# Performance work log

Measured on AMD Instinct MI355X. Metric: run time of the kernel, lower is better.

The kernel has to match this reference:

```python
import jax, jax.numpy as jnp
import numpy as np
import math

B, S, H, DK, NB = 2, 128, 4, 128, 4
D = H * DK  # 512


def setup_inputs() -> dict:
    key = jax.random.key(0)
    ks = jax.random.split(key, 24)
    g = lambda i, sh, std=1.0: jax.random.normal(ks[i], sh, jnp.float32) * std
    u = lambda i, sh: jax.random.uniform(ks[i], sh, jnp.float32)
    return {
        "x_m": g(0, (B, S, D)), "x_c": g(1, (B, S, D)),
        "b_m": g(2, (B, S, D)), "b_c": g(3, (B, S, D)),
        "bb_m": g(4, (B, NB, NB, D)), "bb_c": u(5, (B, NB, NB, D)),
        "p_m": g(6, (B, S, D)), "p_c": u(7, (B, S, D)),
        "W_xm": g(8, (3, D, H, DK), 0.02), "W_xc": g(9, (3, D, H, DK), 0.02),
        "W_bm": g(10, (3, D, H, DK), 0.02), "W_bc": g(11, (3, D, H, DK), 0.02),
        "Wq1_w": g(12, (DK, DK), 0.05), "Wq1_b": g(13, (DK,), 0.02),
        "Wq2_w": g(14, (DK, DK), 0.05), "Wq2_b": g(15, (DK,), 0.02),
        "Wk1_w": g(16, (DK, DK), 0.05), "Wk1_b": g(17, (DK,), 0.02),
        "Wk2_w": g(18, (DK, DK), 0.05), "Wk2_b": g(19, (DK,), 0.02),
        "mean_w": g(20, (D, D), 0.02), "mean_b": jnp.zeros((D,), jnp.float32),
        "cov_w": g(21, (D, D), 0.02), "cov_b": jnp.zeros((D,), jnp.float32),
        "ln_w": jnp.ones((D,), jnp.float32), "ln_b": jnp.zeros((D,), jnp.float32),
        "b_seq": jax.random.randint(ks[22], (B, S), 0, NB),
    }


def _elu1(x):
    return jax.nn.elu(x) + 1.0


def _tri_sagp(m1, m2, m3, c1, c2, c3):
    # fuse three diagonal Gaussians by product-of-Gaussians (precision-weighted)
    eps = 1e-24
    p1 = 1.0 / jnp.clip(c1, eps)
    p2 = 1.0 / jnp.clip(c2, eps)
    p3 = 1.0 / jnp.clip(c3, eps)
    c = 1.0 / (p1 + p2 + p3)
    return c * (m1 * p1 + m2 * p2 + m3 * p3), c


def _ln(x, w, b):
    m = jnp.mean(x, -1, keepdims=True)
    v = jnp.mean((x - m) ** 2, -1, keepdims=True)
    return (x - m) / jnp.sqrt(v + 1e-12) * w + b


def _forward(x_m, x_c, b_m, b_c, bb_m, bb_c, p_m, p_c,
             W_xm, W_xc, W_bm, W_bc,
             Wq1_w, Wq1_b, Wq2_w, Wq2_b, Wk1_w, Wk1_b, Wk2_w, Wk2_b,
             mean_w, mean_b, cov_w, cov_b, ln_w, ln_b, b_seq):
    Bb, Ss, Dd = x_m.shape
    Hh, Dk = W_xm.shape[2], W_xm.shape[3]
    proj = lambda x, w: jnp.einsum('bnd,dhk->bhnk', x, w)
    q1 = proj(x_m, W_xm[0]) + proj(b_m, W_bm[0])
    k1 = proj(x_m, W_xm[1]) + proj(b_m, W_bm[1])
    v1 = proj(x_m, W_xm[2]) + proj(b_m, W_bm[2])
    q2 = _elu1(proj(x_c, W_xc[0]) + proj(b_c, W_bc[0]))
    k2 = _elu1(proj(x_c, W_xc[1]) + proj(b_c, W_bc[1]))
    v2 = _elu1(proj(x_c, W_xc[2]) + proj(b_c, W_bc[2]))
    nb = bb_m.shape[1]
    # [B,NB,NB,D] -> [B,H,NB,NB,DK]
    bbm = bb_m.reshape(Bb, nb, nb, Hh, Dk).transpose(0, 3, 1, 2, 4)
    bbc = bb_c.reshape(Bb, nb, nb, Hh, Dk).transpose(0, 3, 1, 2, 4)
    # out[b,h,i,j,:] = bbm[b,h,b_seq[b,j],b_seq[b,i],:]  (matches torch advanced indexing + permute)
    gather = jax.vmap(lambda bb, seq: bb[:, seq[None, :], seq[:, None], :])
    bbm_b = gather(bbm, b_seq)  # [B,H,S,S,DK]
    bbc_b = gather(bbc, b_seq)
    pm = p_m.reshape(Bb, Ss, Hh, Dk).transpose(0, 2, 1, 3)  # [B,H,S,DK]
    pc = p_c.reshape(Bb, Ss, Hh, Dk).transpose(0, 2, 1, 3)
    lin = lambda x, w, b: x @ w.T + b
    fQm, fQc = _tri_sagp(q1[:, :, :, None, :], lin(bbm_b, Wq1_w, Wq1_b),
                         lin(pm, Wq2_w, Wq2_b)[:, :, :, None, :],
                         q2[:, :, :, None, :], bbc_b, pc[:, :, :, None, :])
    fKm, fKc = _tri_sagp(k1[:, :, None, :, :], lin(bbm_b, Wk1_w, Wk1_b),
                         lin(pm, Wk2_w, Wk2_b)[:, :, None, :, :],
                         k2[:, :, None, :, :], bbc_b, pc[:, :, None, :, :])
    eps = 1e-24
    # 2-Wasserstein^2 between diagonal Gaussians (the 1x1 matmul form reduces to this)
    w2 = jnp.sum((fQm - fKm) ** 2, -1) + jnp.sum(
        (jnp.sqrt(jnp.clip(fQc, eps)) - jnp.sqrt(jnp.clip(fKc, eps))) ** 2, -1)
    scores = -w2 / math.sqrt(Dk)  # [B,H,S,S]
    probs = jax.nn.softmax(scores, axis=-1)
    mean_ctx = jnp.einsum('bhij,bhjk->bhik', probs, v1)
    cov_ctx = jnp.einsum('bhij,bhjk->bhik', probs ** 2, v2)
    mean_ctx = mean_ctx.transpose(0, 2, 1, 3).reshape(Bb, Ss, Dd)
    cov_ctx = cov_ctx.transpose(0, 2, 1, 3).reshape(Bb, Ss, Dd)
    mean_h = _ln(mean_ctx @ mean_w.T + mean_b + x_m, ln_w, ln_b)
    cov_h = _ln(cov_ctx @ cov_w.T + cov_b + x_c, ln_w, ln_b)
    return mean_h, cov_h, probs


def reference(x_m, x_c, b_m, b_c, bb_m, bb_c, p_m, p_c,
              W_xm, W_xc, W_bm, W_bc,
              Wq1_w, Wq1_b, Wq2_w, Wq2_b, Wk1_w, Wk1_b, Wk2_w, Wk2_b,
              mean_w, mean_b, cov_w, cov_b, ln_w, ln_b, b_seq):
    return _forward(x_m, x_c, b_m, b_c, bb_m, bb_c, p_m, p_c,
                    W_xm, W_xc, W_bm, W_bc,
                    Wq1_w, Wq1_b, Wq2_w, Wq2_b, Wk1_w, Wk1_b, Wk2_w, Wk2_b,
                    mean_w, mean_b, cov_w, cov_b, ln_w, ln_b, b_seq)
```

## Files before the change

### kernel.cpp

```cpp
#include <hip/hip_runtime.h>
#include <math.h>

#define B_ 2
#define S_ 128
#define H_ 4
#define DK_ 128
#define NB_ 4
#define D_ 512
#define M_ 256

typedef __attribute__((ext_vector_type(8))) short short8;
typedef __attribute__((ext_vector_type(4))) float float4v;
typedef __attribute__((ext_vector_type(4))) unsigned short ushort4v;

__device__ __forceinline__ float elu1(float x) {
    return (x > 0.f) ? (x + 1.f) : __expf(x);
}

__device__ __forceinline__ unsigned short f2bf(float f) {
    unsigned u = __float_as_uint(f);
    unsigned r = (u + 0x7FFFu + ((u >> 16) & 1u)) >> 16;
    return (unsigned short)r;
}


__global__ __launch_bounds__(256) void k_prep(
    const float* __restrict__ x_m, const float* __restrict__ b_m,
    const float* __restrict__ x_c, const float* __restrict__ b_c,
    const float* __restrict__ mean_w, const float* __restrict__ cov_w,
    const float* __restrict__ W_xm, const float* __restrict__ W_xc,
    const float* __restrict__ W_bm, const float* __restrict__ W_bc,
    const float* __restrict__ p_m, const float* __restrict__ bb_m,
    const float* __restrict__ Wq2, const float* __restrict__ Wk2,
    const float* __restrict__ Wq1, const float* __restrict__ Wk1,
    unsigned short* __restrict__ A_m, unsigned short* __restrict__ A_c,
    unsigned short* __restrict__ wm_bf, unsigned short* __restrict__ wc_bf,
    unsigned short* __restrict__ Wt,
    unsigned short* __restrict__ pm_bf, unsigned short* __restrict__ bbm_bf,
    unsigned short* __restrict__ w4_bf)
{
    __shared__ unsigned short tile4[4][32][33];
    const int t = threadIdx.x;
    const int blk = blockIdx.x;
    const int NBK = gridDim.x;

    for (int cid = blk * 256 + t; cid < 315392; cid += NBK * 256) {
        const float* srcp;
        unsigned short* dstp;
        if (cid < 262144) {
            int job = cid >> 16;
            int off = (cid & 65535) * 4;
            if (job <= 1) {
                int m = off >> 10, k = off & 1023;
                if (job == 0) { srcp = (k < 512) ? (x_m + m * 512 + k) : (b_m + m * 512 + k - 512); dstp = A_m + off; }
                else          { srcp = (k < 512) ? (x_c + m * 512 + k) : (b_c + m * 512 + k - 512); dstp = A_c + off; }
            } else if (job == 2) { srcp = mean_w + off; dstp = wm_bf + off; }
            else                 { srcp = cov_w + off;  dstp = wc_bf + off; }
        } else if (cid < 294912) {
            int off = (cid - 262144) * 4;
            srcp = p_m + off; dstp = pm_bf + off;
        } else if (cid < 299008) {
            int off = (cid - 294912) * 4;
            srcp = bb_m + off; dstp = bbm_bf + off;
        } else {
            int off = (cid - 299008) * 4;
            int seg = off >> 14;
            const float* Ws = (seg == 0) ? Wq2 : (seg == 1) ? Wk2 : (seg == 2) ? Wq1 : Wk1;
            srcp = Ws + (off & 16383); dstp = w4_bf + off;
        }
        float4 v = *(const float4*)srcp;
        ushort4v o4;
        o4.x = f2bf(v.x); o4.y = f2bf(v.y); o4.z = f2bf(v.z); o4.w = f2bf(v.w);
        *(ushort4v*)dstp = o4;
    }

    const int tx = t & 31, ty = t >> 5;
#pragma unroll
    for (int it = 0; it < 4; ++it) {
        int tid = blk + it * 768;
        int nt = tid & 15, kt = (tid >> 4) & 15, z = tid >> 8;
        int o = z >> 1, part = z & 1;
        const float* src;
        if (part == 0) src = (o < 3) ? (W_xm + o * 262144) : (W_xc + (o - 3) * 262144);
        else           src = (o < 3) ? (W_bm + o * 262144) : (W_bc + (o - 3) * 262144);
#pragma unroll
        for (int u = 0; u < 4; ++u)
            tile4[it][ty + u * 8][tx] = f2bf(src[(kt * 32 + ty + u * 8) * 512 + nt * 32 + tx]);
    }
    __syncthreads();
#pragma unroll
    for (int it = 0; it < 4; ++it) {
        int tid = blk + it * 768;
        int nt = tid & 15, kt = (tid >> 4) & 15, z = tid >> 8;
        int o = z >> 1, part = z & 1;
        unsigned short* dst = Wt + o * 524288 + part * 512;
#pragma unroll
        for (int u = 0; u < 4; ++u)
            dst[(nt * 32 + ty + u * 8) * 1024 + kt * 32 + tx] = tile4[it][tx][ty + u * 8];
    }
}

__global__ __launch_bounds__(256) void k_mm(
    const unsigned short* __restrict__ A_m, const unsigned short* __restrict__ A_c,
    const unsigned short* __restrict__ Wt,
    const unsigned short* __restrict__ pm_bf, const unsigned short* __restrict__ bbm_bf,
    const unsigned short* __restrict__ w4_bf,
    const float* __restrict__ bq2, const float* __restrict__ bk2,
    const float* __restrict__ bq1, const float* __restrict__ bk1,
    float* __restrict__ qkv, float* __restrict__ pq, float* __restrict__ pk,
    float* __restrict__ bbq, float* __restrict__ bbk)
{
    const int t = threadIdx.x;
    const int blk = blockIdx.x;
    const int sblk = (blk < 384) ? ((blk & 7) * 48 + (blk >> 3)) : blk;
    const int wid = sblk * 4 + (t >> 6);
    const int lane = t & 63;
    const int l15 = lane & 15, quad = lane >> 4;

    if (wid < 1536) {
        const int o = wid >> 8;
        const int rem = wid & 255;
        const int nt2 = rem & 15, mt = rem >> 4;
        const int m0 = mt * 16, n0 = nt2 * 32;

        const unsigned short* A = (o < 3) ? A_m : A_c;
        const unsigned short* ap  = A + (m0 + l15) * 1024 + quad * 8;
        const unsigned short* bpa = Wt + o * 524288 + (n0 + l15) * 1024 + quad * 8;
        const unsigned short* bpb = bpa + 16 * 1024;

        float4v accA0 = {0.f, 0.f, 0.f, 0.f};
        float4v accA1 = {0.f, 0.f, 0.f, 0.f};
        float4v accB0 = {0.f, 0.f, 0.f, 0.f};
        float4v accB1 = {0.f, 0.f, 0.f, 0.f};
#pragma unroll
        for (int k0 = 0; k0 < 1024; k0 += 64) {
            short8 a0 = *(const short8*)(ap + k0);
            short8 a1 = *(const short8*)(ap + k0 + 32);
            short8 b0a = *(const short8*)(bpa + k0);
            short8 b1a = *(const short8*)(bpa + k0 + 32);
            short8 b0b = *(const short8*)(bpb + k0);
            short8 b1b = *(const short8*)(bpb + k0 + 32);
            accA0 = __builtin_amdgcn_mfma_f32_16x16x32_bf16(a0, b0a, accA0, 0, 0, 0);
            accA1 = __builtin_amdgcn_mfma_f32_16x16x32_bf16(a1, b1a, accA1, 0, 0, 0);
            accB0 = __builtin_amdgcn_mfma_f32_16x16x32_bf16(a0, b0b, accB0, 0, 0, 0);
            accB1 = __builtin_amdgcn_mfma_f32_16x16x32_bf16(a1, b1b, accB1, 0, 0, 0);
        }
        float* dst = qkv + o * 131072;
#pragma unroll
        for (int r = 0; r < 4; ++r) {
            float va = accA0[r] + accA1[r];
            float vb = accB0[r] + accB1[r];
            if (o >= 3) { va = elu1(va); vb = elu1(vb); }
            dst[(m0 + quad * 4 + r) * 512 + n0 + l15] = va;
            dst[(m0 + quad * 4 + r) * 512 + n0 + 16 + l15] = vb;
        }
    } else {
        const unsigned short* Abf;
        const unsigned short* Wb;
        const float* bias;
        float* dst;
        int m0, n0, h;
        if (wid < 2560) {
            int lid = wid - 1536;
            int sel = lid >> 9;
            int r = lid & 511;
            h = r >> 7;
            int rem = r & 127;
            m0 = (rem >> 3) * 16; n0 = (rem & 7) * 16;
            Abf = pm_bf;
            Wb = w4_bf + sel * 16384;
            bias = sel ? bk2 : bq2;
            dst = sel ? pk : pq;
        } else {
            int lid = wid - 2560;
            int sel = lid >> 6;
            int r = lid & 63;
            h = r >> 4;
            int rem = r & 15;
            m0 = (rem >> 3) * 16; n0 = (rem & 7) * 16;
            Abf = bbm_bf;
            Wb = w4_bf + 32768 + sel * 16384;
            bias = sel ? bk1 : bq1;
            dst = sel ? bbk : bbq;
        }
        const unsigned short* ap = Abf + (m0 + l15) * 512 + h * 128 + quad * 8;
        const unsigned short* bp = Wb + (n0 + l15) * 128 + quad * 8;

        float4v acc0 = {0.f, 0.f, 0.f, 0.f};
        float4v acc1 = {0.f, 0.f, 0.f, 0.f};
#pragma unroll
        for (int k0 = 0; k0 < 128; k0 += 64) {
            short8 a0 = *(const short8*)(ap + k0);
            short8 b0 = *(const short8*)(bp + k0);
            short8 a1 = *(const short8*)(ap + k0 + 32);
            short8 b1 = *(const short8*)(bp + k0 + 32);
            acc0 = __builtin_amdgcn_mfma_f32_16x16x32_bf16(a0, b0, acc0, 0, 0, 0);
            acc1 = __builtin_amdgcn_mfma_f32_16x16x32_bf16(a1, b1, acc1, 0, 0, 0);
        }
        float bv = bias[n0 + l15];
#pragma unroll
        for (int r = 0; r < 4; ++r)
            dst[(m0 + quad * 4 + r) * 512 + h * 128 + n0 + l15] = acc0[r] + acc1[r] + bv;
    }
}

__global__ __launch_bounds__(128) void k_fuseK(
    const float* __restrict__ qkv, const float* __restrict__ pk,
    const float* __restrict__ bbk, const float* __restrict__ bb_c,
    const float* __restrict__ p_c, const int* __restrict__ b_seq,
    float* __restrict__ fKm, float* __restrict__ fKs)
{
    const int t = threadIdx.x;
    const int j = blockIdx.x, h = blockIdx.y, b = blockIdx.z;
    const int d = h * 128 + t;
    const float eps = 1e-24f;
    const int base = (b * S_ + j) * D_ + d;
    const int sj = b_seq[b * S_ + j];

    float m1 = qkv[M_ * D_ + base];
    float c1 = qkv[4 * M_ * D_ + base];
    float m3 = pk[base];
    float c3 = p_c[base];

    float p1 = 1.f / fmaxf(c1, eps);
    float p3 = 1.f / fmaxf(c3, eps);
    float mp13 = m1 * p1 + m3 * p3;

#pragma unroll
    for (int sv = 0; sv < 4; ++sv) {
        int idx = (b * 16 + sj * 4 + sv) * 512 + d;
        float m2 = bbk[idx];
        float c2 = bb_c[idx];
        float p2 = 1.f / fmaxf(c2, eps);
        float cc = 1.f / (p1 + p2 + p3);
        int o = (((b * H_ + h) * 4 + sv) * S_ + j) * 128 + t;
        fKm[o] = cc * (mp13 + m2 * p2);
        fKs[o] = sqrtf(fmaxf(cc, eps));
    }
}

__global__ __launch_bounds__(128) void k_attn3(
    const float* __restrict__ qkv, const float* __restrict__ pq,
    const float* __restrict__ bbq, const float* __restrict__ bb_c,
    const float* __restrict__ p_c, const int* __restrict__ b_seq,
    const float* __restrict__ fKm, const float* __restrict__ fKs,
    float* __restrict__ probs_out, unsigned short* __restrict__ mctxb,
    unsigned short* __restrict__ cctxb)
{
    const int t = threadIdx.x;
    const int blk = blockIdx.x;
    const int bh = blk & 7;
    const int i = blk >> 3;
    const int b = bh >> 2, h = bh & 3;
    const float eps = 1e-24f;

    __shared__ __attribute__((aligned(16))) float qm[4 * 132];
    __shared__ __attribute__((aligned(16))) float qs[4 * 132];
    __shared__ float red[4];
    __shared__ float pr[128], pr2[128];

    const int si = b_seq[b * S_ + i];
    const int sj = b_seq[b * S_ + t];

    {
        const int d = h * 128 + t;
        const int base = (b * S_ + i) * D_ + d;
        float m1 = qkv[base];
        float c1 = qkv[3 * M_ * D_ + base];
        float m3 = pq[base];
        float c3 = p_c[base];
        float p1 = 1.f / fmaxf(c1, eps);
        float p3 = 1.f / fmaxf(c3, eps);
        float mp13 = m1 * p1 + m3 * p3;
#pragma unroll
        for (int sv = 0; sv < 4; ++sv) {
            int idx = (b * 16 + sv * 4 + si) * 512 + d;
            float m2 = bbq[idx];
            float c2 = bb_c[idx];
            float p2 = 1.f / fmaxf(c2, eps);
            float cc = 1.f / (p1 + p2 + p3);
            qm[sv * 132 + t] = cc * (mp13 + m2 * p2);
            qs[sv * 132 + t] = sqrtf(fmaxf(cc, eps));
        }
    }
    __syncthreads();

    const int krow = (((b * H_ + h) * 4 + si) * S_ + t) * 128;
    const float4* kmp = (const float4*)(fKm + krow);
    const float4* ksp = (const float4*)(fKs + krow);

    float w2 = 0.f;
#pragma unroll 4
    for (int k4 = 0; k4 < 32; ++k4) {
        float4 km = kmp[k4];
        float4 ks = ksp[k4];
        float4 m = *(const float4*)&qm[sj * 132 + k4 * 4];
        float4 s = *(const float4*)&qs[sj * 132 + k4 * 4];
        float d0 = m.x - km.x, d1 = m.y - km.y, d2 = m.z - km.z, d3 = m.w - km.w;
        float e0 = s.x - ks.x, e1 = s.y - ks.y, e2 = s.z - ks.z, e3 = s.w - ks.w;
        w2 += d0 * d0 + d1 * d1 + d2 * d2 + d3 * d3
            + e0 * e0 + e1 * e1 + e2 * e2 + e3 * e3;
    }
    float score = -w2 * 0.08838834764831845f;

    float mx = score;
#pragma unroll
    for (int off = 32; off >= 1; off >>= 1) mx = fmaxf(mx, __shfl_xor(mx, off));
    if ((t & 63) == 0) red[t >> 6] = mx;
    __syncthreads();
    mx = fmaxf(red[0], red[1]);
    float e = __expf(score - mx);
    float sm = e;
#pragma unroll
    for (int off = 32; off >= 1; off >>= 1) sm += __shfl_xor(sm, off);
    if ((t & 63) == 0) red[2 + (t >> 6)] = sm;
    __syncthreads();
    float p = e / (red[2] + red[3]);

    probs_out[((b * H_ + h) * S_ + i) * S_ + t] = p;
    pr[t] = p;
    pr2[t] = p * p;
    __syncthreads();

    const float* v1 = qkv + 2 * M_ * D_ + (b * S_) * D_ + h * 128 + t;
    const float* v2 = qkv + 5 * M_ * D_ + (b * S_) * D_ + h * 128 + t;
    float am = 0.f, ac = 0.f;
#pragma unroll 8
    for (int j = 0; j < 128; ++j) {
        am = fmaf(pr[j], v1[j * D_], am);
        ac = fmaf(pr2[j], v2[j * D_], ac);
    }
    mctxb[(b * S_ + i) * D_ + h * 128 + t] = f2bf(am);
    cctxb[(b * S_ + i) * D_ + h * 128 + t] = f2bf(ac);
}

__global__ __launch_bounds__(256) void k_fin_mm(
    const unsigned short* __restrict__ mctxb, const unsigned short* __restrict__ cctxb,
    const unsigned short* __restrict__ wm_bf, const unsigned short* __restrict__ wc_bf,
    float* __restrict__ y_m, float* __restrict__ y_c)
{
    const int t = threadIdx.x;
    const int wid = blockIdx.x * 4 + (t >> 6);
    const int lane = t & 63;
    const int mat = wid >> 9;
    const int rem = wid & 511;
    const int nt = rem & 31, mt = rem >> 5;
    const int m0 = mt * 16, n0 = nt * 16;
    const int l15 = lane & 15, quad = lane >> 4;

    const unsigned short* A = mat ? cctxb : mctxb;
    const unsigned short* Bw = mat ? wc_bf : wm_bf;
    float* y = mat ? y_c : y_m;

    const unsigned short* ap = A + (m0 + l15) * 512 + quad * 8;
    const unsigned short* bp = Bw + (n0 + l15) * 512 + quad * 8;

    float4v acc0 = {0.f, 0.f, 0.f, 0.f};
    float4v acc1 = {0.f, 0.f, 0.f, 0.f};
#pragma unroll
    for (int k0 = 0; k0 < 512; k0 += 64) {
        short8 a0 = *(const short8*)(ap + k0);
        short8 b0 = *(const short8*)(bp + k0);
        short8 a1 = *(const short8*)(ap + k0 + 32);
        short8 b1 = *(const short8*)(bp + k0 + 32);
        acc0 = __builtin_amdgcn_mfma_f32_16x16x32_bf16(a0, b0, acc0, 0, 0, 0);
        acc1 = __builtin_amdgcn_mfma_f32_16x16x32_bf16(a1, b1, acc1, 0, 0, 0);
    }
#pragma unroll
    for (int r = 0; r < 4; ++r)
        y[(m0 + quad * 4 + r) * 512 + n0 + l15] = acc0[r] + acc1[r];
}

__global__ __launch_bounds__(256) void k_ln(
    const float* __restrict__ y_m, const float* __restrict__ y_c,
    const float* __restrict__ mean_b, const float* __restrict__ cov_b,
    const float* __restrict__ x_m, const float* __restrict__ x_c,
    const float* __restrict__ ln_w, const float* __restrict__ ln_b,
    float* __restrict__ out)
{
    const int t = threadIdx.x;
    const int id = blockIdx.x;
    const int mat = id >> 8, row = id & 255;
    const float* yg = mat ? y_c : y_m;
    const float* bias = mat ? cov_b : mean_b;
    const float* res = mat ? x_c : x_m;
    const int base = row * 512;

    __shared__ float red[8];

    float y0 = yg[base + t] + bias[t] + res[base + t];
    float y1 = yg[base + 256 + t] + bias[256 + t] + res[base + 256 + t];
    float s = y0 + y1, ss = y0 * y0 + y1 * y1;
#pragma unroll
    for (int off = 32; off >= 1; off >>= 1) { s += __shfl_xor(s, off); ss += __shfl_xor(ss, off); }
    if ((t & 63) == 0) { red[t >> 6] = s; red[4 + (t >> 6)] = ss; }
    __syncthreads();
    float mu = (red[0] + red[1] + red[2] + red[3]) * (1.f / 512.f);
    float var = (red[4] + red[5] + red[6] + red[7]) * (1.f / 512.f) - mu * mu;
    float rstd = 1.f / sqrtf(var + 1e-12f);
    out[mat * 131072 + base + t] = (y0 - mu) * rstd * ln_w[t] + ln_b[t];
    out[mat * 131072 + base + 256 + t] = (y1 - mu) * rstd * ln_w[256 + t] + ln_b[256 + t];
}

extern "C" void kernel_launch(void* const* d_in, const int* in_sizes, int n_in,
                              void* d_out, int out_size, void* d_ws, size_t ws_size,
                              hipStream_t stream) {
    (void)in_sizes; (void)n_in; (void)out_size; (void)ws_size;
    const float* x_m   = (const float*)d_in[0];
    const float* x_c   = (const float*)d_in[1];
    const float* b_m   = (const float*)d_in[2];
    const float* b_c   = (const float*)d_in[3];
    const float* bb_m  = (const float*)d_in[4];
    const float* bb_c  = (const float*)d_in[5];
    const float* p_m   = (const float*)d_in[6];
    const float* p_c   = (const float*)d_in[7];
    const float* W_xm  = (const float*)d_in[8];
    const float* W_xc  = (const float*)d_in[9];
    const float* W_bm  = (const float*)d_in[10];
    const float* W_bc  = (const float*)d_in[11];
    const float* Wq1_w = (const float*)d_in[12];
    const float* Wq1_b = (const float*)d_in[13];
    const float* Wq2_w = (const float*)d_in[14];
    const float* Wq2_b = (const float*)d_in[15];
    const float* Wk1_w = (const float*)d_in[16];
    const float* Wk1_b = (const float*)d_in[17];
    const float* Wk2_w = (const float*)d_in[18];
    const float* Wk2_b = (const float*)d_in[19];
    const float* mean_w = (const float*)d_in[20];
    const float* mean_b = (const float*)d_in[21];
    const float* cov_w  = (const float*)d_in[22];
    const float* cov_b  = (const float*)d_in[23];
    const float* ln_w   = (const float*)d_in[24];
    const float* ln_b   = (const float*)d_in[25];
    const int*   b_seq  = (const int*)d_in[26];

    float* ws = (float*)d_ws;
    float* qkv = ws;
    float* pq  = ws + 786432;
    float* pk  = ws + 917504;
    float* bbq = ws + 1048576;
    float* bbk = ws + 1064960;
    float* fKm = ws + 1081344;
    float* fKs = ws + 1605632;
    float* y_m = ws + 2129920;
    float* y_c = ws + 2260992;
    unsigned short* A_m    = (unsigned short*)(ws + 2392064);
    unsigned short* A_c    = (unsigned short*)(ws + 2523136);
    unsigned short* Wt     = (unsigned short*)(ws + 2654208);
    unsigned short* wm_bf  = (unsigned short*)(ws + 4227072);
    unsigned short* wc_bf  = (unsigned short*)(ws + 4358144);
    unsigned short* mctxb  = (unsigned short*)(ws + 4489216);
    unsigned short* cctxb  = (unsigned short*)(ws + 4554752);
    unsigned short* pm_bf  = (unsigned short*)(ws + 4620288);
    unsigned short* bbm_bf = (unsigned short*)(ws + 4685824);
    unsigned short* w4_bf  = (unsigned short*)(ws + 4694016);
    float* out = (float*)d_out;

    k_prep<<<dim3(768), 256, 0, stream>>>(
        x_m, b_m, x_c, b_c, mean_w, cov_w, W_xm, W_xc, W_bm, W_bc,
        p_m, bb_m, Wq2_w, Wk2_w, Wq1_w, Wk1_w,
        A_m, A_c, wm_bf, wc_bf, Wt, pm_bf, bbm_bf, w4_bf);
    k_mm<<<dim3(672), 256, 0, stream>>>(
        A_m, A_c, Wt, pm_bf, bbm_bf, w4_bf,
        Wq2_b, Wk2_b, Wq1_b, Wk1_b,
        qkv, pq, pk, bbq, bbk);
    k_fuseK<<<dim3(128, 4, 2), 128, 0, stream>>>(
        qkv, pk, bbk, bb_c, p_c, b_seq, fKm, fKs);
    k_attn3<<<dim3(1024), 128, 0, stream>>>(
        qkv, pq, bbq, bb_c, p_c, b_seq, fKm, fKs, out + 262144, mctxb, cctxb);
    k_fin_mm<<<dim3(256), 256, 0, stream>>>(
        mctxb, cctxb, wm_bf, wc_bf, y_m, y_c);
    k_ln<<<dim3(512), 256, 0, stream>>>(
        y_m, y_c, mean_b, cov_b, x_m, x_c, ln_w, ln_b, out);
}
```

Before: 176.2 us.

## Fuse six kernel launches into one cooperative persistent kernel with grid syncs

Replaces the six-kernel pipeline (prep, projection matmuls, key fusion, attention, output matmul, layernorm) with one cooperative kernel of 512 blocks. Stages are separated by grid-wide syncs, and each stage's work is remapped onto the fixed grid. This aims to remove per-launch overhead and inter-kernel gaps. In exchange it adds grid-barrier cost and limits parallelism to 512 blocks, with the old launches kept as a fallback if the cooperative launch fails.

```diff
diff --git a/kernel.cpp b/kernel.cpp
--- a/kernel.cpp
+++ b/kernel.cpp
@@ -1,5 +1,8 @@
 #include <hip/hip_runtime.h>
+#include <hip/hip_cooperative_groups.h>
 #include <math.h>
+
+namespace cg = cooperative_groups;
 
 #define B_ 2
 #define S_ 128
@@ -21,6 +24,360 @@
     unsigned u = __float_as_uint(f);
     unsigned r = (u + 0x7FFFu + ((u >> 16) & 1u)) >> 16;
     return (unsigned short)r;
+}
+
+
+struct MegaArgs {
+    const float *x_m, *x_c, *b_m, *b_c, *bb_m, *bb_c, *p_m, *p_c;
+    const float *W_xm, *W_xc, *W_bm, *W_bc;
+    const float *Wq1_b, *Wq2_w, *Wq2_b, *Wk1_b, *Wk2_w, *Wk2_b;
+    const float *Wq1_w, *Wk1_w;
+    const float *mean_w, *mean_b, *cov_w, *cov_b, *ln_w, *ln_b;
+    const int *b_seq;
+    float *qkv, *pq, *pk, *bbq, *bbk, *fKm, *fKs, *y_m, *y_c;
+    unsigned short *A_m, *A_c, *Wt, *wm_bf, *wc_bf, *mctxb, *cctxb, *pm_bf, *bbm_bf, *w4_bf;
+    float *out;
+};
+
+__global__ __launch_bounds__(256) void k_mega(MegaArgs P)
+{
+    cg::grid_group gg = cg::this_grid();
+    __shared__ __attribute__((aligned(16))) float smemf[2640];
+    const int t = threadIdx.x;
+    const int blk = blockIdx.x;
+
+    for (int cid = blk * 256 + t; cid < 315392; cid += 131072) {
+        const float* srcp;
+        unsigned short* dstp;
+        if (cid < 262144) {
+            int job = cid >> 16;
+            int off = (cid & 65535) * 4;
+            if (job <= 1) {
+                int m = off >> 10, k = off & 1023;
+                if (job == 0) { srcp = (k < 512) ? (P.x_m + m * 512 + k) : (P.b_m + m * 512 + k - 512); dstp = P.A_m + off; }
+                else          { srcp = (k < 512) ? (P.x_c + m * 512 + k) : (P.b_c + m * 512 + k - 512); dstp = P.A_c + off; }
+            } else if (job == 2) { srcp = P.mean_w + off; dstp = P.wm_bf + off; }
+            else                 { srcp = P.cov_w + off;  dstp = P.wc_bf + off; }
+        } else if (cid < 294912) {
+            int off = (cid - 262144) * 4;
+            srcp = P.p_m + off; dstp = P.pm_bf + off;
+        } else if (cid < 299008) {
+            int off = (cid - 294912) * 4;
+            srcp = P.bb_m + off; dstp = P.bbm_bf + off;
+        } else {
+            int off = (cid - 299008) * 4;
+            int seg = off >> 14;
+            const float* Ws = (seg == 0) ? P.Wq2_w : (seg == 1) ? P.Wk2_w : (seg == 2) ? P.Wq1_w : P.Wk1_w;
+            srcp = Ws + (off & 16383); dstp = P.w4_bf + off;
+        }
+        float4 v = *(const float4*)srcp;
+        ushort4v o4;
+        o4.x = f2bf(v.x); o4.y = f2bf(v.y); o4.z = f2bf(v.z); o4.w = f2bf(v.w);
+        *(ushort4v*)dstp = o4;
+    }
+
+    {
+        unsigned short (*tile2)[32][33] = reinterpret_cast<unsigned short(*)[32][33]>(smemf);
+        const int tx = t & 31, ty = t >> 5;
+        for (int batch = 0; batch < 3; ++batch) {
+            __syncthreads();
+#pragma unroll
+            for (int it = 0; it < 2; ++it) {
+                const int tid = blk + (batch * 2 + it) * 512;
+                const int nt = tid & 15, kt = (tid >> 4) & 15, z = tid >> 8;
+                const int o = z >> 1, part = z & 1;
+                const float* src = (part == 0)
+                    ? ((o < 3) ? (P.W_xm + o * 262144) : (P.W_xc + (o - 3) * 262144))
+                    : ((o < 3) ? (P.W_bm + o * 262144) : (P.W_bc + (o - 3) * 262144));
+#pragma unroll
+                for (int u = 0; u < 4; ++u)
+                    tile2[it][ty + u * 8][tx] = f2bf(src[(kt * 32 + ty + u * 8) * 512 + nt * 32 + tx]);
+            }
+            __syncthreads();
+#pragma unroll
+            for (int it = 0; it < 2; ++it) {
+                const int tid = blk + (batch * 2 + it) * 512;
+                const int nt = tid & 15, kt = (tid >> 4) & 15, z = tid >> 8;
+                const int o = z >> 1, part = z & 1;
+                unsigned short* dst = P.Wt + o * 524288 + part * 512;
+#pragma unroll
+                for (int u = 0; u < 4; ++u)
+                    dst[(nt * 32 + ty + u * 8) * 1024 + kt * 32 + tx] = tile2[it][tx][ty + u * 8];
+            }
+        }
+    }
+    gg.sync();
+
+    {
+        const int lane = t & 63;
+        const int l15 = lane & 15, quad = lane >> 4;
+        for (int wid = blk * 4 + (t >> 6); wid < 2688; wid += 2048) {
+            if (wid < 1536) {
+                const int o = wid >> 8;
+                const int rem = wid & 255;
+                const int nt2 = rem & 15, mt = rem >> 4;
+                const int m0 = mt * 16, n0 = nt2 * 32;
+
+                const unsigned short* Abf = (o < 3) ? P.A_m : P.A_c;
+                const unsigned short* ap  = Abf + (m0 + l15) * 1024 + quad * 8;
+                const unsigned short* bpa = P.Wt + o * 524288 + (n0 + l15) * 1024 + quad * 8;
+                const unsigned short* bpb = bpa + 16 * 1024;
+
+                float4v accA0 = {0.f, 0.f, 0.f, 0.f};
+                float4v accA1 = {0.f, 0.f, 0.f, 0.f};
+                float4v accB0 = {0.f, 0.f, 0.f, 0.f};
+                float4v accB1 = {0.f, 0.f, 0.f, 0.f};
+#pragma unroll
+                for (int k0 = 0; k0 < 1024; k0 += 64) {
+                    short8 a0 = *(const short8*)(ap + k0);
+                    short8 a1 = *(const short8*)(ap + k0 + 32);
+                    short8 b0a = *(const short8*)(bpa + k0);
+                    short8 b1a = *(const short8*)(bpa + k0 + 32);
+                    short8 b0b = *(const short8*)(bpb + k0);
+                    short8 b1b = *(const short8*)(bpb + k0 + 32);
+                    accA0 = __builtin_amdgcn_mfma_f32_16x16x32_bf16(a0, b0a, accA0, 0, 0, 0);
+                    accA1 = __builtin_amdgcn_mfma_f32_16x16x32_bf16(a1, b1a, accA1, 0, 0, 0);
+                    accB0 = __builtin_amdgcn_mfma_f32_16x16x32_bf16(a0, b0b, accB0, 0, 0, 0);
+                    accB1 = __builtin_amdgcn_mfma_f32_16x16x32_bf16(a1, b1b, accB1, 0, 0, 0);
+                }
+                float* dst = P.qkv + o * 131072;
+#pragma unroll
+                for (int r = 0; r < 4; ++r) {
+                    float va = accA0[r] + accA1[r];
+                    float vb = accB0[r] + accB1[r];
+                    if (o >= 3) { va = elu1(va); vb = elu1(vb); }
+                    dst[(m0 + quad * 4 + r) * 512 + n0 + l15] = va;
+                    dst[(m0 + quad * 4 + r) * 512 + n0 + 16 + l15] = vb;
+                }
+            } else {
+                const unsigned short* Abf;
+                const unsigned short* Wb;
+                const float* bias;
+                float* dst;
+                int m0, n0, h;
+                if (wid < 2560) {
+                    int lid = wid - 1536;
+                    int sel = lid >> 9;
+                    int r = lid & 511;
+                    h = r >> 7;
+                    int rem = r & 127;
+                    m0 = (rem >> 3) * 16; n0 = (rem & 7) * 16;
+                    Abf = P.pm_bf;
+                    Wb = P.w4_bf + sel * 16384;
+                    bias = sel ? P.Wk2_b : P.Wq2_b;
+                    dst = sel ? P.pk : P.pq;
+                } else {
+                    int lid = wid - 2560;
+                    int sel = lid >> 6;
+                    int r = lid & 63;
+                    h = r >> 4;
+                    int rem = r & 15;
+                    m0 = (rem >> 3) * 16; n0 = (rem & 7) * 16;
+                    Abf = P.bbm_bf;
+                    Wb = P.w4_bf + 32768 + sel * 16384;
+                    bias = sel ? P.Wk1_b : P.Wq1_b;
+                    dst = sel ? P.bbk : P.bbq;
+                }
+                const unsigned short* ap = Abf + (m0 + l15) * 512 + h * 128 + quad * 8;
+                const unsigned short* bp = Wb + (n0 + l15) * 128 + quad * 8;
+
+                float4v acc0 = {0.f, 0.f, 0.f, 0.f};
+                float4v acc1 = {0.f, 0.f, 0.f, 0.f};
+#pragma unroll
+                for (int k0 = 0; k0 < 128; k0 += 64) {
+                    short8 a0 = *(const short8*)(ap + k0);
+                    short8 b0 = *(const short8*)(bp + k0);
+                    short8 a1 = *(const short8*)(ap + k0 + 32);
+                    short8 b1 = *(const short8*)(bp + k0 + 32);
+                    acc0 = __builtin_amdgcn_mfma_f32_16x16x32_bf16(a0, b0, acc0, 0, 0, 0);
+                    acc1 = __builtin_amdgcn_mfma_f32_16x16x32_bf16(a1, b1, acc1, 0, 0, 0);
+                }
+                float bv = bias[n0 + l15];
+#pragma unroll
+                for (int r = 0; r < 4; ++r)
+                    dst[(m0 + quad * 4 + r) * 512 + h * 128 + n0 + l15] = acc0[r] + acc1[r] + bv;
+            }
+        }
+    }
+    gg.sync();
+
+    {
+        const int half = t >> 7, tl = t & 127;
+        const int u = blk * 2 + half;
+        const int j = u & 127, h = (u >> 7) & 3, b = u >> 9;
+        const float eps = 1e-24f;
+        const int d = h * 128 + tl;
+        const int base = (b * S_ + j) * D_ + d;
+        const int sj = P.b_seq[b * S_ + j];
+
+        float m1 = P.qkv[M_ * D_ + base];
+        float c1 = P.qkv[4 * M_ * D_ + base];
+        float m3 = P.pk[base];
+        float c3 = P.p_c[base];
+
+        float p1 = 1.f / fmaxf(c1, eps);
+        float p3 = 1.f / fmaxf(c3, eps);
+        float mp13 = m1 * p1 + m3 * p3;
+
+#pragma unroll
+        for (int sv = 0; sv < 4; ++sv) {
+            int idx = (b * 16 + sj * 4 + sv) * 512 + d;
+            float m2 = P.bbk[idx];
+            float c2 = P.bb_c[idx];
+            float p2 = 1.f / fmaxf(c2, eps);
+            float cc = 1.f / (p1 + p2 + p3);
+            int o = (((b * H_ + h) * 4 + sv) * S_ + j) * 128 + tl;
+            P.fKm[o] = cc * (mp13 + m2 * p2);
+            P.fKs[o] = sqrtf(fmaxf(cc, eps));
+        }
+    }
+    gg.sync();
+
+    {
+        const int half = t >> 7, tl = t & 127;
+        const int u = blk * 2 + half;
+        const int i = u & 127, h = (u >> 7) & 3, b = u >> 9;
+        const float eps = 1e-24f;
+
+        float* qm  = smemf + half * 528;
+        float* qs  = smemf + 1056 + half * 528;
+        float* pr  = smemf + 2112 + half * 128;
+        float* pr2 = smemf + 2368 + half * 128;
+        float* red = smemf + 2624 + half * 4;
+
+        const int si = P.b_seq[b * S_ + i];
+        const int sj = P.b_seq[b * S_ + tl];
+
+        {
+            const int d = h * 128 + tl;
+            const int base = (b * S_ + i) * D_ + d;
+            float m1 = P.qkv[base];
+            float c1 = P.qkv[3 * M_ * D_ + base];
+            float m3 = P.pq[base];
+            float c3 = P.p_c[base];
+            float p1 = 1.f / fmaxf(c1, eps);
+            float p3 = 1.f / fmaxf(c3, eps);
+            float mp13 = m1 * p1 + m3 * p3;
+#pragma unroll
+            for (int sv = 0; sv < 4; ++sv) {
+                int idx = (b * 16 + sv * 4 + si) * 512 + d;
+                float m2 = P.bbq[idx];
+                float c2 = P.bb_c[idx];
+                float p2 = 1.f / fmaxf(c2, eps);
+                float cc = 1.f / (p1 + p2 + p3);
+                qm[sv * 132 + tl] = cc * (mp13 + m2 * p2);
+                qs[sv * 132 + tl] = sqrtf(fmaxf(cc, eps));
+            }
+        }
+        __syncthreads();
+
+        const int krow = (((b * H_ + h) * 4 + si) * S_ + tl) * 128;
+        const float4* kmp = (const float4*)(P.fKm + krow);
+        const float4* ksp = (const float4*)(P.fKs + krow);
+
+        float w2 = 0.f;
+#pragma unroll 4
+        for (int k4 = 0; k4 < 32; ++k4) {
+            float4 km = kmp[k4];
+            float4 ks = ksp[k4];
+            float4 m = *(const float4*)&qm[sj * 132 + k4 * 4];
+            float4 s = *(const float4*)&qs[sj * 132 + k4 * 4];
+            float d0 = m.x - km.x, d1 = m.y - km.y, d2 = m.z - km.z, d3 = m.w - km.w;
+            float e0 = s.x - ks.x, e1 = s.y - ks.y, e2 = s.z - ks.z, e3 = s.w - ks.w;
+            w2 += d0 * d0 + d1 * d1 + d2 * d2 + d3 * d3
+                + e0 * e0 + e1 * e1 + e2 * e2 + e3 * e3;
+        }
+        float score = -w2 * 0.08838834764831845f;
+
+        float mx = score;
+#pragma unroll
+        for (int off = 32; off >= 1; off >>= 1) mx = fmaxf(mx, __shfl_xor(mx, off));
+        if ((tl & 63) == 0) red[tl >> 6] = mx;
+        __syncthreads();
+        mx = fmaxf(red[0], red[1]);
+        float e = __expf(score - mx);
+        float sm = e;
+#pragma unroll
+        for (int off = 32; off >= 1; off >>= 1) sm += __shfl_xor(sm, off);
+        if ((tl & 63) == 0) red[2 + (tl >> 6)] = sm;
+        __syncthreads();
+        float p = e / (red[2] + red[3]);
+
+        P.out[262144 + ((b * H_ + h) * S_ + i) * S_ + tl] = p;
+        pr[tl] = p;
+        pr2[tl] = p * p;
+        __syncthreads();
+
+        const float* v1 = P.qkv + 2 * M_ * D_ + (b * S_) * D_ + h * 128 + tl;
+        const float* v2 = P.qkv + 5 * M_ * D_ + (b * S_) * D_ + h * 128 + tl;
+        float am = 0.f, ac = 0.f;
+#pragma unroll 8
+        for (int j = 0; j < 128; ++j) {
+            am = fmaf(pr[j], v1[j * D_], am);
+            ac = fmaf(pr2[j], v2[j * D_], ac);
+        }
+        P.mctxb[(b * S_ + i) * D_ + h * 128 + tl] = f2bf(am);
+        P.cctxb[(b * S_ + i) * D_ + h * 128 + tl] = f2bf(ac);
+    }
+    gg.sync();
+
+    {
+        const int lane = t & 63;
+        const int l15 = lane & 15, quad = lane >> 4;
+        const int wid = blk * 4 + (t >> 6);
+        if (wid < 1024) {
+            const int mat = wid >> 9;
+            const int rem = wid & 511;
+            const int nt = rem & 31, mt = rem >> 5;
+            const int m0 = mt * 16, n0 = nt * 16;
+
+            const unsigned short* Ap = mat ? P.cctxb : P.mctxb;
+            const unsigned short* Bw = mat ? P.wc_bf : P.wm_bf;
+            float* y = mat ? P.y_c : P.y_m;
+
+            const unsigned short* ap = Ap + (m0 + l15) * 512 + quad * 8;
+            const unsigned short* bp = Bw + (n0 + l15) * 512 + quad * 8;
+
+            float4v acc0 = {0.f, 0.f, 0.f, 0.f};
+            float4v acc1 = {0.f, 0.f, 0.f, 0.f};
+#pragma unroll
+            for (int k0 = 0; k0 < 512; k0 += 64) {
+                short8 a0 = *(const short8*)(ap + k0);
+                short8 b0 = *(const short8*)(bp + k0);
+                short8 a1 = *(const short8*)(ap + k0 + 32);
+                short8 b1 = *(const short8*)(bp + k0 + 32);
+                acc0 = __builtin_amdgcn_mfma_f32_16x16x32_bf16(a0, b0, acc0, 0, 0, 0);
+                acc1 = __builtin_amdgcn_mfma_f32_16x16x32_bf16(a1, b1, acc1, 0, 0, 0);
+            }
+#pragma unroll
+            for (int r = 0; r < 4; ++r)
+                y[(m0 + quad * 4 + r) * 512 + n0 + l15] = acc0[r] + acc1[r];
+        }
+    }
+    gg.sync();
+
+    {
+        float* red8 = smemf;
+        const int id = blk;
+        const int mat = id >> 8, row = id & 255;
+        const float* yg = mat ? P.y_c : P.y_m;
+        const float* bias = mat ? P.cov_b : P.mean_b;
+        const float* res = mat ? P.x_c : P.x_m;
+        const int base = row * 512;
+
+        float y0 = yg[base + t] + bias[t] + res[base + t];
+        float y1 = yg[base + 256 + t] + bias[256 + t] + res[base + 256 + t];
+        float s = y0 + y1, ss = y0 * y0 + y1 * y1;
+#pragma unroll
+        for (int off = 32; off >= 1; off >>= 1) { s += __shfl_xor(s, off); ss += __shfl_xor(ss, off); }
+        if ((t & 63) == 0) { red8[t >> 6] = s; red8[4 + (t >> 6)] = ss; }
+        __syncthreads();
+        float mu = (red8[0] + red8[1] + red8[2] + red8[3]) * (1.f / 512.f);
+        float var = (red8[4] + red8[5] + red8[6] + red8[7]) * (1.f / 512.f) - mu * mu;
+        float rstd = 1.f / sqrtf(var + 1e-12f);
+        P.out[mat * 131072 + base + t] = (y0 - mu) * rstd * P.ln_w[t] + P.ln_b[t];
+        P.out[mat * 131072 + base + 256 + t] = (y1 - mu) * rstd * P.ln_w[256 + t] + P.ln_b[256 + t];
+    }
 }
 
 
@@ -456,20 +813,43 @@
     unsigned short* w4_bf  = (unsigned short*)(ws + 4694016);
     float* out = (float*)d_out;
 
-    k_prep<<<dim3(768), 256, 0, stream>>>(
-        x_m, b_m, x_c, b_c, mean_w, cov_w, W_xm, W_xc, W_bm, W_bc,
-        p_m, bb_m, Wq2_w, Wk2_w, Wq1_w, Wk1_w,
-        A_m, A_c, wm_bf, wc_bf, Wt, pm_bf, bbm_bf, w4_bf);
-    k_mm<<<dim3(672), 256, 0, stream>>>(
-        A_m, A_c, Wt, pm_bf, bbm_bf, w4_bf,
-        Wq2_b, Wk2_b, Wq1_b, Wk1_b,
-        qkv, pq, pk, bbq, bbk);
-    k_fuseK<<<dim3(128, 4, 2), 128, 0, stream>>>(
-        qkv, pk, bbk, bb_c, p_c, b_seq, fKm, fKs);
-    k_attn3<<<dim3(1024), 128, 0, stream>>>(
-        qkv, pq, bbq, bb_c, p_c, b_seq, fKm, fKs, out + 262144, mctxb, cctxb);
-    k_fin_mm<<<dim3(256), 256, 0, stream>>>(
-        mctxb, cctxb, wm_bf, wc_bf, y_m, y_c);
-    k_ln<<<dim3(512), 256, 0, stream>>>(
-        y_m, y_c, mean_b, cov_b, x_m, x_c, ln_w, ln_b, out);
-}
+    MegaArgs ma;
+    ma.x_m = x_m; ma.x_c = x_c; ma.b_m = b_m; ma.b_c = b_c;
+    ma.bb_m = bb_m; ma.bb_c = bb_c; ma.p_m = p_m; ma.p_c = p_c;
+    ma.W_xm = W_xm; ma.W_xc = W_xc; ma.W_bm = W_bm; ma.W_bc = W_bc;
+    ma.Wq1_b = Wq1_b; ma.Wq2_w = Wq2_w; ma.Wq2_b = Wq2_b;
+    ma.Wk1_b = Wk1_b; ma.Wk2_w = Wk2_w; ma.Wk2_b = Wk2_b;
+    ma.Wq1_w = Wq1_w; ma.Wk1_w = Wk1_w;
+    ma.mean_w = mean_w; ma.mean_b = mean_b; ma.cov_w = cov_w; ma.cov_b = cov_b;
+    ma.ln_w = ln_w; ma.ln_b = ln_b; ma.b_seq = b_seq;
+    ma.qkv = qkv; ma.pq = pq; ma.pk = pk; ma.bbq = bbq; ma.bbk = bbk;
+    ma.fKm = fKm; ma.fKs = fKs; ma.y_m = y_m; ma.y_c = y_c;
+    ma.A_m = A_m; ma.A_c = A_c; ma.Wt = Wt; ma.wm_bf = wm_bf; ma.wc_bf = wc_bf;
+    ma.mctxb = mctxb; ma.cctxb = cctxb; ma.pm_bf = pm_bf; ma.bbm_bf = bbm_bf;
+    ma.w4_bf = w4_bf; ma.out = out;
+
+    void* kargs[] = { (void*)&ma };
+    hipError_t err = hipLaunchCooperativeKernel(
+        reinterpret_cast<const void*>(&k_mega), dim3(512), dim3(256),
+        kargs, 0, stream);
+
+    if (err != hipSuccess) {
+        (void)hipGetLastError();
+        k_prep<<<dim3(768), 256, 0, stream>>>(
+            x_m, b_m, x_c, b_c, mean_w, cov_w, W_xm, W_xc, W_bm, W_bc,
+            p_m, bb_m, Wq2_w, Wk2_w, Wq1_w, Wk1_w,
+            A_m, A_c, wm_bf, wc_bf, Wt, pm_bf, bbm_bf, w4_bf);
+        k_mm<<<dim3(672), 256, 0, stream>>>(
+            A_m, A_c, Wt, pm_bf, bbm_bf, w4_bf,
+            Wq2_b, Wk2_b, Wq1_b, Wk1_b,
+            qkv, pq, pk, bbq, bbk);
+        k_fuseK<<<dim3(128, 4, 2), 128, 0, stream>>>(
+            qkv, pk, bbk, bb_c, p_c, b_seq, fKm, fKs);
+        k_attn3<<<dim3(1024), 128, 0, stream>>>(
+            qkv, pq, bbq, bb_c, p_c, b_seq, fKm, fKs, out + 262144, mctxb, cctxb);
+        k_fin_mm<<<dim3(256), 256, 0, stream>>>(
+            mctxb, cctxb, wm_bf, wc_bf, y_m, y_c);
+        k_ln<<<dim3(512), 256, 0, stream>>>(
+            y_m, y_c, mean_b, cov_b, x_m, x_c, ln_w, ln_b, out);
+    }
+}
```

New measurement: 485.4 us. 2.76x slower.

## Fuse final output projection GEMM with residual add and LayerNorm

Applied to the files above, without the earlier changes.

Merges the output-projection MFMA GEMM and the LayerNorm kernel into one kernel. Each block computes a full 16-row by 512-column tile into shared memory, then applies bias, residual and LayerNorm per row. This removes one launch and the global round trip of the intermediate y buffers. The cost is a grid of only 32 blocks with 8 serial tiles per wave, which leaves most of the chip idle during the GEMM.

```diff
diff --git a/kernel.cpp b/kernel.cpp
--- a/kernel.cpp
+++ b/kernel.cpp
@@ -334,72 +334,77 @@
     cctxb[(b * S_ + i) * D_ + h * 128 + t] = f2bf(ac);
 }
 
-__global__ __launch_bounds__(256) void k_fin_mm(
+__global__ __launch_bounds__(256) void k_finln(
     const unsigned short* __restrict__ mctxb, const unsigned short* __restrict__ cctxb,
     const unsigned short* __restrict__ wm_bf, const unsigned short* __restrict__ wc_bf,
-    float* __restrict__ y_m, float* __restrict__ y_c)
-{
-    const int t = threadIdx.x;
-    const int wid = blockIdx.x * 4 + (t >> 6);
-    const int lane = t & 63;
-    const int mat = wid >> 9;
-    const int rem = wid & 511;
-    const int nt = rem & 31, mt = rem >> 5;
-    const int m0 = mt * 16, n0 = nt * 16;
-    const int l15 = lane & 15, quad = lane >> 4;
-
-    const unsigned short* A = mat ? cctxb : mctxb;
-    const unsigned short* Bw = mat ? wc_bf : wm_bf;
-    float* y = mat ? y_c : y_m;
-
-    const unsigned short* ap = A + (m0 + l15) * 512 + quad * 8;
-    const unsigned short* bp = Bw + (n0 + l15) * 512 + quad * 8;
-
-    float4v acc0 = {0.f, 0.f, 0.f, 0.f};
-    float4v acc1 = {0.f, 0.f, 0.f, 0.f};
-#pragma unroll
-    for (int k0 = 0; k0 < 512; k0 += 64) {
-        short8 a0 = *(const short8*)(ap + k0);
-        short8 b0 = *(const short8*)(bp + k0);
-        short8 a1 = *(const short8*)(ap + k0 + 32);
-        short8 b1 = *(const short8*)(bp + k0 + 32);
-        acc0 = __builtin_amdgcn_mfma_f32_16x16x32_bf16(a0, b0, acc0, 0, 0, 0);
-        acc1 = __builtin_amdgcn_mfma_f32_16x16x32_bf16(a1, b1, acc1, 0, 0, 0);
-    }
-#pragma unroll
-    for (int r = 0; r < 4; ++r)
-        y[(m0 + quad * 4 + r) * 512 + n0 + l15] = acc0[r] + acc1[r];
-}
-
-__global__ __launch_bounds__(256) void k_ln(
-    const float* __restrict__ y_m, const float* __restrict__ y_c,
     const float* __restrict__ mean_b, const float* __restrict__ cov_b,
     const float* __restrict__ x_m, const float* __restrict__ x_c,
     const float* __restrict__ ln_w, const float* __restrict__ ln_b,
     float* __restrict__ out)
 {
     const int t = threadIdx.x;
-    const int id = blockIdx.x;
-    const int mat = id >> 8, row = id & 255;
-    const float* yg = mat ? y_c : y_m;
+    const int blk = blockIdx.x;
+    const int mat = blk >> 4;
+    const int rg  = blk & 15;
+    const int m0 = rg * 16;
+    const int w = t >> 6;
+    const int lane = t & 63;
+    const int l15 = lane & 15, quad = lane >> 4;
+
+    __shared__ __attribute__((aligned(16))) float ytile[16][512];
+
+    const unsigned short* A  = mat ? cctxb : mctxb;
+    const unsigned short* Bw = mat ? wc_bf : wm_bf;
+
+    const unsigned short* ap = A + (m0 + l15) * 512 + quad * 8;
+
+#pragma unroll 2
+    for (int j = 0; j < 8; ++j) {
+        const int n0 = (w * 8 + j) * 16;
+        const unsigned short* bp = Bw + (n0 + l15) * 512 + quad * 8;
+        float4v acc0 = {0.f, 0.f, 0.f, 0.f};
+        float4v acc1 = {0.f, 0.f, 0.f, 0.f};
+#pragma unroll
+        for (int k0 = 0; k0 < 512; k0 += 64) {
+            short8 a0 = *(const short8*)(ap + k0);
+            short8 b0 = *(const short8*)(bp + k0);
+            short8 a1 = *(const short8*)(ap + k0 + 32);
+            short8 b1 = *(const short8*)(bp + k0 + 32);
+            acc0 = __builtin_amdgcn_mfma_f32_16x16x32_bf16(a0, b0, acc0, 0, 0, 0);
+            acc1 = __builtin_amdgcn_mfma_f32_16x16x32_bf16(a1, b1, acc1, 0, 0, 0);
+        }
+#pragma unroll
+        for (int r = 0; r < 4; ++r)
+            ytile[quad * 4 + r][n0 + l15] = acc0[r] + acc1[r];
+    }
+    __syncthreads();
+
     const float* bias = mat ? cov_b : mean_b;
-    const float* res = mat ? x_c : x_m;
-    const int base = row * 512;
-
-    __shared__ float red[8];
-
-    float y0 = yg[base + t] + bias[t] + res[base + t];
-    float y1 = yg[base + 256 + t] + bias[256 + t] + res[base + 256 + t];
-    float s = y0 + y1, ss = y0 * y0 + y1 * y1;
-#pragma unroll
-    for (int off = 32; off >= 1; off >>= 1) { s += __shfl_xor(s, off); ss += __shfl_xor(ss, off); }
-    if ((t & 63) == 0) { red[t >> 6] = s; red[4 + (t >> 6)] = ss; }
-    __syncthreads();
-    float mu = (red[0] + red[1] + red[2] + red[3]) * (1.f / 512.f);
-    float var = (red[4] + red[5] + red[6] + red[7]) * (1.f / 512.f) - mu * mu;
-    float rstd = 1.f / sqrtf(var + 1e-12f);
-    out[mat * 131072 + base + t] = (y0 - mu) * rstd * ln_w[t] + ln_b[t];
-    out[mat * 131072 + base + 256 + t] = (y1 - mu) * rstd * ln_w[256 + t] + ln_b[256 + t];
+    const float* res  = mat ? x_c : x_m;
+#pragma unroll
+    for (int rr = 0; rr < 4; ++rr) {
+        const int row = w * 4 + rr;
+        const int base = (m0 + row) * 512;
+        const int c0 = lane * 8;
+        float v[8];
+        float s = 0.f, ss = 0.f;
+#pragma unroll
+        for (int c = 0; c < 8; ++c) {
+            float y = ytile[row][c0 + c] + bias[c0 + c] + res[base + c0 + c];
+            v[c] = y; s += y; ss += y * y;
+        }
+#pragma unroll
+        for (int off = 32; off >= 1; off >>= 1) {
+            s += __shfl_xor(s, off);
+            ss += __shfl_xor(ss, off);
+        }
+        float mu = s * (1.f / 512.f);
+        float var = ss * (1.f / 512.f) - mu * mu;
+        float rstd = 1.f / sqrtf(var + 1e-12f);
+#pragma unroll
+        for (int c = 0; c < 8; ++c)
+            out[mat * 131072 + base + c0 + c] = (v[c] - mu) * rstd * ln_w[c0 + c] + ln_b[c0 + c];
+    }
 }
 
 extern "C" void kernel_launch(void* const* d_in, const int* in_sizes, int n_in,
@@ -442,8 +447,6 @@
     float* bbk = ws + 1064960;
     float* fKm = ws + 1081344;
     float* fKs = ws + 1605632;
-    float* y_m = ws + 2129920;
-    float* y_c = ws + 2260992;
     unsigned short* A_m    = (unsigned short*)(ws + 2392064);
     unsigned short* A_c    = (unsigned short*)(ws + 2523136);
     unsigned short* Wt     = (unsigned short*)(ws + 2654208);
@@ -468,8 +471,6 @@
         qkv, pk, bbk, bb_c, p_c, b_seq, fKm, fKs);
     k_attn3<<<dim3(1024), 128, 0, stream>>>(
         qkv, pq, bbq, bb_c, p_c, b_seq, fKm, fKs, out + 262144, mctxb, cctxb);
-    k_fin_mm<<<dim3(256), 256, 0, stream>>>(
-        mctxb, cctxb, wm_bf, wc_bf, y_m, y_c);
-    k_ln<<<dim3(512), 256, 0, stream>>>(
-        y_m, y_c, mean_b, cov_b, x_m, x_c, ln_w, ln_b, out);
-}
+    k_finln<<<dim3(32), 256, 0, stream>>>(
+        mctxb, cctxb, wm_bf, wc_bf, mean_b, cov_b, x_m, x_c, ln_w, ln_b, out);
+}
```

Result: slower. 187.4 us (+6.4%).
